# Kernel optimization log

Measured on AMD Instinct MI355X. Metric: run time of the kernel, lower is better.

## Reference

```python
import jax, jax.numpy as jnp
import numpy as np

B, C, N, K = 2, 64, 65536, 16
OUT = 64


def setup_inputs() -> dict:
    key = jax.random.key(0)
    k1, k2, k3, k4 = jax.random.split(key, 4)
    x = jax.random.normal(k1, (B, C, N, 1), dtype=jnp.float32)
    edge_index = jax.random.randint(k2, (2, B, N, K), 0, N, dtype=jnp.int64)
    # 1x1 conv weight of MLP2dLayer([2*C, OUT]) and its bias
    W = jax.random.normal(k3, (OUT, 2 * C), dtype=jnp.float32) * (1.0 / np.sqrt(2 * C))
    b = jax.random.normal(k4, (OUT,), dtype=jnp.float32) * 0.01
    return {"x": x, "edge_index": edge_index, "W": W, "b": b}


def reference(x, edge_index, W, b):
    # x: [B, C, N, 1], edge_index: [2, B, N, K]
    Bs, Cs, Ns, _ = x.shape
    Ks = edge_index.shape[-1]
    feat = x[..., 0]                                   # [B, C, N]
    idx = edge_index[0].reshape(Bs, 1, Ns * Ks)        # [B, 1, N*K]
    idx = jnp.broadcast_to(idx, (Bs, Cs, Ns * Ks))
    x_j = jnp.take_along_axis(feat, idx, axis=2).reshape(Bs, Cs, Ns, Ks)  # gather neighbors
    x_i = jnp.broadcast_to(x[..., :1], (Bs, Cs, Ns, Ks))                  # repeated center feature
    msg = jnp.concatenate([x_i, x_j - x_i], axis=1)    # [B, 2C, N, K]
    h = jnp.einsum("oi,bink->bonk", W, msg) + b[None, :, None, None]
    h = jax.nn.relu(h)                                 # MLP2dLayer: 1x1 conv + relu (norm=None)
    out = jnp.max(h, axis=-1, keepdims=True)           # max aggregation over neighbors
    return out
```

## Files before the change

### kernel.cpp

```cpp
#include <hip/hip_runtime.h>


using u32 = unsigned int;
using u16 = unsigned short;
typedef short short8 __attribute__((ext_vector_type(8)));
typedef float f32x4 __attribute__((ext_vector_type(4)));
typedef int i32x4 __attribute__((ext_vector_type(4)));
typedef u32 u32x4 __attribute__((ext_vector_type(4)));

#define NN 65536

static __device__ __forceinline__ u16 bf16r(float a) {
  u32 u = __builtin_bit_cast(u32, a);
  return (u16)((u + 0x7fffu + ((u >> 16) & 1u)) >> 16);
}
static __device__ __forceinline__ u32 pack_bf16(float a, float b) {
  return (u32)bf16r(a) | ((u32)bf16r(b) << 16);
}
static __device__ __forceinline__ float bflo(u32 x) {
  return __builtin_bit_cast(float, x << 16);
}
static __device__ __forceinline__ float bfhi(u32 x) {
  return __builtin_bit_cast(float, x & 0xffff0000u);
}

__global__ __launch_bounds__(256) void prep_w(const float* __restrict__ W,
                                              u32* __restrict__ Wcat) {
  int id = blockIdx.x * 256 + threadIdx.x;
  int o = id >> 5, c2 = id & 31;
  float f0, f1;
  if (o < 64) {
    f0 = W[o * 128 + 2 * c2]     - W[o * 128 + 64 + 2 * c2];
    f1 = W[o * 128 + 2 * c2 + 1] - W[o * 128 + 64 + 2 * c2 + 1];
  } else {
    int om = o - 64;
    f0 = W[om * 128 + 64 + 2 * c2];
    f1 = W[om * 128 + 64 + 2 * c2 + 1];
  }
  Wcat[id] = pack_bf16(f0, f1);
}

__global__ __launch_bounds__(256, 4) void k1(const float* __restrict__ x,
                                             const float* __restrict__ bias,
                                             const u32* __restrict__ Wcat,
                                             u32* __restrict__ Up,
                                             u32* __restrict__ Vp) {
  __shared__ __align__(16) char smem[26880];
  u32* Wb = (u32*)smem;
  u32* Xa = (u32*)(smem + 18432);

  int t = threadIdx.x;
  int l = t & 63;
  int w = t >> 6;
  int b = blockIdx.x >> 10;
  int n0 = (blockIdx.x & 1023) << 6;

#pragma unroll
  for (int i = 0; i < 16; ++i) {
    int id = i * 256 + t;
    Wb[(id >> 5) * 36 + (id & 31)] = Wcat[id];
  }
#pragma unroll
  for (int r = 0; r < 8; ++r) {
    int c2 = r * 4 + w;
    size_t base = ((size_t)(b * 64 + 2 * c2)) * NN + n0 + l;
    Xa[l * 33 + c2] = pack_bf16(x[base], x[base + NN]);
  }
  __syncthreads();

  f32x4 acc[8];
#pragma unroll
  for (int f = 0; f < 8; ++f) acc[f] = {0.f, 0.f, 0.f, 0.f};

#pragma unroll
  for (int kb = 0; kb < 2; ++kb) {
    int ar = (16 * w + (l & 15)) * 33 + kb * 16 + 4 * (l >> 4);
    i32x4 av = {(int)Xa[ar], (int)Xa[ar + 1], (int)Xa[ar + 2], (int)Xa[ar + 3]};
    short8 a = __builtin_bit_cast(short8, av);
#pragma unroll
    for (int f = 0; f < 8; ++f) {
      i32x4 bv = *(const i32x4*)(Wb + (16 * f + (l & 15)) * 36 + kb * 16 + 4 * (l >> 4));
      short8 bb = __builtin_bit_cast(short8, bv);
      acc[f] = __builtin_amdgcn_mfma_f32_16x16x32_bf16(a, bb, acc[f], 0, 0, 0);
    }
  }

  float bs[4];
#pragma unroll
  for (int f = 0; f < 4; ++f) bs[f] = bias[16 * f + (l & 15)];

  __syncthreads();
  u16* TR16 = (u16*)smem;
#pragma unroll
  for (int f = 0; f < 4; ++f) {
#pragma unroll
    for (int r = 0; r < 4; ++r) {
      int node = 16 * w + 4 * (l >> 4) + r;
      int o = 16 * f + (l & 15);
      float uval = acc[f][r] + bs[f];
      float vval = acc[f + 4][r];
      TR16[node * 136 + o] = bf16r(uval);
      TR16[node * 136 + 64 + o] = bf16r(vval);
    }
  }
  __syncthreads();

  u32* TR32 = (u32*)smem;
  int o2 = t & 63;
#pragma unroll
  for (int i = 0; i < 16; ++i) {
    int n = i * 4 + w;
    u32 v = TR32[n * 68 + o2];
    size_t node = (size_t)(n0 + n);
    if (o2 < 32) {
      int hh = o2 >> 4, c = o2 & 15;
      Up[(((size_t)hh * 2 + b) * NN + node) * 16 + c] = v;
    } else {
      int o2v = o2 - 32;
      int hh = o2v >> 4, c = o2v & 15;
      Vp[(((size_t)hh * 2 + b) * NN + node) * 16 + c] = v;
    }
  }
}

__global__ __launch_bounds__(256, 8) void k2(const int* __restrict__ eidx,
                                             const u32* __restrict__ Uh,
                                             const u32* __restrict__ Vh,
                                             float* __restrict__ out) {
  __shared__ __align__(16) int eixT[16 * 65];
  __shared__ __align__(16) float tile[32 * 65];

  int t = threadIdx.x;
  int bx = blockIdx.x;
  int xcd = bx & 7;
  int g = xcd >> 1;
  int hh = g >> 1;
  int b = g & 1;
  int n0 = ((bx >> 3) | ((xcd & 1) << 9)) << 6;

  {
    i32x4 v = __builtin_nontemporal_load(
        (const i32x4*)(eidx + ((size_t)b * NN + n0) * 16) + t);
    int node = t >> 2, e0 = (t & 3) * 4;
    eixT[(e0 + 0) * 65 + node] = v.x;
    eixT[(e0 + 1) * 65 + node] = v.y;
    eixT[(e0 + 2) * 65 + node] = v.z;
    eixT[(e0 + 3) * 65 + node] = v.w;
  }
  __syncthreads();

  int l = t & 63, w = t >> 6;
  int node = w * 16 + (l >> 2);
  int qq = l & 3;

  const u32* Vb = Vh + (((size_t)hh * 2 + b) * NN) * 16 + qq * 4;
  float mx[8];
#pragma unroll
  for (int i = 0; i < 8; ++i) mx[i] = -3.0e38f;

#pragma unroll
  for (int e = 0; e < 16; ++e) {
    int id = eixT[e * 65 + node];
    u32x4 v = *(const u32x4*)(Vb + (size_t)id * 16);
    mx[0] = fmaxf(mx[0], bflo(v.x)); mx[1] = fmaxf(mx[1], bfhi(v.x));
    mx[2] = fmaxf(mx[2], bflo(v.y)); mx[3] = fmaxf(mx[3], bfhi(v.y));
    mx[4] = fmaxf(mx[4], bflo(v.z)); mx[5] = fmaxf(mx[5], bfhi(v.z));
    mx[6] = fmaxf(mx[6], bflo(v.w)); mx[7] = fmaxf(mx[7], bfhi(v.w));
  }

  u32x4 uv = __builtin_nontemporal_load(
      (const u32x4*)(Uh + (((size_t)hh * 2 + b) * NN + n0 + node) * 16 + qq * 4));
  tile[(qq * 8 + 0) * 65 + node] = fmaxf(bflo(uv.x) + mx[0], 0.f);
  tile[(qq * 8 + 1) * 65 + node] = fmaxf(bfhi(uv.x) + mx[1], 0.f);
  tile[(qq * 8 + 2) * 65 + node] = fmaxf(bflo(uv.y) + mx[2], 0.f);
  tile[(qq * 8 + 3) * 65 + node] = fmaxf(bfhi(uv.y) + mx[3], 0.f);
  tile[(qq * 8 + 4) * 65 + node] = fmaxf(bflo(uv.z) + mx[4], 0.f);
  tile[(qq * 8 + 5) * 65 + node] = fmaxf(bfhi(uv.z) + mx[5], 0.f);
  tile[(qq * 8 + 6) * 65 + node] = fmaxf(bflo(uv.w) + mx[6], 0.f);
  tile[(qq * 8 + 7) * 65 + node] = fmaxf(bfhi(uv.w) + mx[7], 0.f);
  __syncthreads();

#pragma unroll
  for (int r = 0; r < 8; ++r) {
    int o = r * 4 + (t >> 6);
    int col = t & 63;
    __builtin_nontemporal_store(
        tile[o * 65 + col],
        out + ((size_t)(b * 64 + hh * 32 + o)) * NN + n0 + col);
  }
}

extern "C" void kernel_launch(void* const* d_in, const int* in_sizes, int n_in,
                              void* d_out, int out_size, void* d_ws, size_t ws_size,
                              hipStream_t stream) {
  const float* x = (const float*)d_in[0];
  const int* eidx = (const int*)d_in[1];
  const float* W = (const float*)d_in[2];
  const float* bias = (const float*)d_in[3];

  u32* Up = (u32*)d_ws;
  u32* Vp = Up + (size_t)4 * NN * 16;
  u32* Wcat = (u32*)((char*)d_ws + (size_t)32 * 1024 * 1024);

  prep_w<<<16, 256, 0, stream>>>(W, Wcat);
  k1<<<2 * 1024, 256, 0, stream>>>(x, bias, Wcat, Up, Vp);
  k2<<<4 * 1024, 256, 0, stream>>>(eidx, Up, Vp, (float*)d_out);
}
```

Measured before the change: 53.92 us.

## Split U/V intermediates into 16-channel quarters so each XCD gathers a smaller slice

The intermediate U/V buffers are re-laid out as four 16-channel quarters of 32 bytes per node, instead of two 32-channel halves of 64 bytes. k2 now processes 128 nodes per block with two threads per node, and the low three block-index bits select one (quarter, batch) slice. That pins each XCD to a single 2 MB gather slice, which should fit in its L2 and raise hit rates on the random neighbor gathers. The trade-off is that edge indices are now read four times instead of twice, and the padded shared-memory stride may cause some bank conflicts.

Result: slower. 74.22 us (+37.6%).

```diff
diff --git a/kernel.cpp b/kernel.cpp
--- a/kernel.cpp
+++ b/kernel.cpp
@@ -113,12 +113,12 @@
     u32 v = TR32[n * 68 + o2];
     size_t node = (size_t)(n0 + n);
     if (o2 < 32) {
-      int hh = o2 >> 4, c = o2 & 15;
-      Up[(((size_t)hh * 2 + b) * NN + node) * 16 + c] = v;
+      int q = o2 >> 3, c = o2 & 7;
+      Up[(((size_t)q * 2 + b) * NN + node) * 8 + c] = v;
     } else {
       int o2v = o2 - 32;
-      int hh = o2v >> 4, c = o2v & 15;
-      Vp[(((size_t)hh * 2 + b) * NN + node) * 16 + c] = v;
+      int q = o2v >> 3, c = o2v & 7;
+      Vp[(((size_t)q * 2 + b) * NN + node) * 8 + c] = v;
     }
   }
 }
@@ -127,41 +127,44 @@
                                              const u32* __restrict__ Uh,
                                              const u32* __restrict__ Vh,
                                              float* __restrict__ out) {
-  __shared__ __align__(16) int eixT[16 * 65];
-  __shared__ __align__(16) float tile[32 * 65];
+  __shared__ __align__(16) int eixT[16 * 136];
+  __shared__ __align__(16) float tile[16 * 136];
 
   int t = threadIdx.x;
   int bx = blockIdx.x;
-  int xcd = bx & 7;
-  int g = xcd >> 1;
-  int hh = g >> 1;
+  int g = bx & 7;
+  int q = g >> 1;
   int b = g & 1;
-  int n0 = ((bx >> 3) | ((xcd & 1) << 9)) << 6;
+  int n0 = (bx >> 3) << 7;
 
   {
-    i32x4 v = __builtin_nontemporal_load(
-        (const i32x4*)(eidx + ((size_t)b * NN + n0) * 16) + t);
+    const i32x4* ep = (const i32x4*)(eidx + ((size_t)b * NN + n0) * 16);
+    i32x4 v0 = __builtin_nontemporal_load(ep + t);
+    i32x4 v1 = __builtin_nontemporal_load(ep + t + 256);
     int node = t >> 2, e0 = (t & 3) * 4;
-    eixT[(e0 + 0) * 65 + node] = v.x;
-    eixT[(e0 + 1) * 65 + node] = v.y;
-    eixT[(e0 + 2) * 65 + node] = v.z;
-    eixT[(e0 + 3) * 65 + node] = v.w;
-  }
-  __syncthreads();
-
-  int l = t & 63, w = t >> 6;
-  int node = w * 16 + (l >> 2);
-  int qq = l & 3;
-
-  const u32* Vb = Vh + (((size_t)hh * 2 + b) * NN) * 16 + qq * 4;
+    eixT[(e0 + 0) * 136 + node] = v0.x;
+    eixT[(e0 + 1) * 136 + node] = v0.y;
+    eixT[(e0 + 2) * 136 + node] = v0.z;
+    eixT[(e0 + 3) * 136 + node] = v0.w;
+    eixT[(e0 + 0) * 136 + 64 + node] = v1.x;
+    eixT[(e0 + 1) * 136 + 64 + node] = v1.y;
+    eixT[(e0 + 2) * 136 + 64 + node] = v1.z;
+    eixT[(e0 + 3) * 136 + 64 + node] = v1.w;
+  }
+  __syncthreads();
+
+  int node = t >> 1;
+  int qq = t & 1;
+
+  const u32* Vb = Vh + (((size_t)q * 2 + b) * NN) * 8 + qq * 4;
   float mx[8];
 #pragma unroll
   for (int i = 0; i < 8; ++i) mx[i] = -3.0e38f;
 
 #pragma unroll
   for (int e = 0; e < 16; ++e) {
-    int id = eixT[e * 65 + node];
-    u32x4 v = *(const u32x4*)(Vb + (size_t)id * 16);
+    int id = eixT[e * 136 + node];
+    u32x4 v = *(const u32x4*)(Vb + (size_t)id * 8);
     mx[0] = fmaxf(mx[0], bflo(v.x)); mx[1] = fmaxf(mx[1], bfhi(v.x));
     mx[2] = fmaxf(mx[2], bflo(v.y)); mx[3] = fmaxf(mx[3], bfhi(v.y));
     mx[4] = fmaxf(mx[4], bflo(v.z)); mx[5] = fmaxf(mx[5], bfhi(v.z));
@@ -169,24 +172,25 @@
   }
 
   u32x4 uv = __builtin_nontemporal_load(
-      (const u32x4*)(Uh + (((size_t)hh * 2 + b) * NN + n0 + node) * 16 + qq * 4));
-  tile[(qq * 8 + 0) * 65 + node] = fmaxf(bflo(uv.x) + mx[0], 0.f);
-  tile[(qq * 8 + 1) * 65 + node] = fmaxf(bfhi(uv.x) + mx[1], 0.f);
-  tile[(qq * 8 + 2) * 65 + node] = fmaxf(bflo(uv.y) + mx[2], 0.f);
-  tile[(qq * 8 + 3) * 65 + node] = fmaxf(bfhi(uv.y) + mx[3], 0.f);
-  tile[(qq * 8 + 4) * 65 + node] = fmaxf(bflo(uv.z) + mx[4], 0.f);
-  tile[(qq * 8 + 5) * 65 + node] = fmaxf(bfhi(uv.z) + mx[5], 0.f);
-  tile[(qq * 8 + 6) * 65 + node] = fmaxf(bflo(uv.w) + mx[6], 0.f);
-  tile[(qq * 8 + 7) * 65 + node] = fmaxf(bfhi(uv.w) + mx[7], 0.f);
-  __syncthreads();
-
+      (const u32x4*)(Uh + (((size_t)q * 2 + b) * NN + n0 + node) * 8 + qq * 4));
+  tile[(qq * 8 + 0) * 136 + node] = fmaxf(bflo(uv.x) + mx[0], 0.f);
+  tile[(qq * 8 + 1) * 136 + node] = fmaxf(bfhi(uv.x) + mx[1], 0.f);
+  tile[(qq * 8 + 2) * 136 + node] = fmaxf(bflo(uv.y) + mx[2], 0.f);
+  tile[(qq * 8 + 3) * 136 + node] = fmaxf(bfhi(uv.y) + mx[3], 0.f);
+  tile[(qq * 8 + 4) * 136 + node] = fmaxf(bflo(uv.z) + mx[4], 0.f);
+  tile[(qq * 8 + 5) * 136 + node] = fmaxf(bfhi(uv.z) + mx[5], 0.f);
+  tile[(qq * 8 + 6) * 136 + node] = fmaxf(bflo(uv.w) + mx[6], 0.f);
+  tile[(qq * 8 + 7) * 136 + node] = fmaxf(bfhi(uv.w) + mx[7], 0.f);
+  __syncthreads();
+
+  int col = t & 127;
+  int oh = t >> 7;
 #pragma unroll
   for (int r = 0; r < 8; ++r) {
-    int o = r * 4 + (t >> 6);
-    int col = t & 63;
+    int o = r * 2 + oh;
     __builtin_nontemporal_store(
-        tile[o * 65 + col],
-        out + ((size_t)(b * 64 + hh * 32 + o)) * NN + n0 + col);
+        tile[o * 136 + col],
+        out + ((size_t)(b * 64 + q * 16 + o)) * NN + n0 + col);
   }
 }
 
@@ -199,7 +203,7 @@
   const float* bias = (const float*)d_in[3];
 
   u32* Up = (u32*)d_ws;
-  u32* Vp = Up + (size_t)4 * NN * 16;
+  u32* Vp = Up + (size_t)8 * NN * 8;
   u32* Wcat = (u32*)((char*)d_ws + (size_t)32 * 1024 * 1024);
 
   prep_w<<<16, 256, 0, stream>>>(W, Wcat);
```
